# Kernel tuning notes

Hardware: AMD Instinct MI355X
Metric: run time of the kernel (lower is better)

The kernel has to match this reference:

```python
import jax, jax.numpy as jnp
import numpy as np

N = 16384      # total nodes
B = 8          # graphs in batch
NPG = N // B   # nodes per graph
E = 262144     # edges
IN, HID, OUT = 128, 256, 128
ICP_ITERS = 10


def setup_inputs():
    key = jax.random.key(0)
    ks = jax.random.split(key, 12)
    x = jax.random.normal(ks[0], (N, IN), jnp.float32)
    # random edges kept within each graph (offsets per graph)
    src = jax.random.randint(ks[1], (E,), 0, NPG, dtype=jnp.int32)
    dst = jax.random.randint(ks[2], (E,), 0, NPG, dtype=jnp.int32)
    goff = (jnp.arange(E, dtype=jnp.int32) % B) * NPG
    edge_index = jnp.stack([src + goff, dst + goff], 0)
    pos = jax.random.normal(ks[3], (N, 3), jnp.float32)
    batch = jnp.repeat(jnp.arange(B, dtype=jnp.int32), NPG)
    def lin(k, fi, fo):
        return jax.random.normal(k, (fi, fo), jnp.float32) * (fi ** -0.5)
    return dict(
        x=x, edge_index=edge_index, pos=pos, batch=batch,
        W1=lin(ks[4], IN, HID),  b1=jnp.zeros((HID,), jnp.float32),
        W2=lin(ks[5], HID, HID), b2=jnp.zeros((HID,), jnp.float32),
        W3=lin(ks[6], HID, OUT), b3=jnp.zeros((OUT,), jnp.float32),
        Wt=lin(ks[7], OUT, 3),   bt=jnp.zeros((3,), jnp.float32),
    )


def gcn_conv(x, W, b, row, col, n):
    # GCNConv: symmetric norm with self loops; messages flow row->col
    xw = x @ W
    loop = jnp.arange(n, dtype=row.dtype)
    r = jnp.concatenate([row, loop])
    c = jnp.concatenate([col, loop])
    deg = jax.ops.segment_sum(jnp.ones_like(c, dtype=xw.dtype), c, num_segments=n)
    dinv = jnp.where(deg > 0, jax.lax.rsqrt(jnp.maximum(deg, 1e-12)), 0.0)
    norm = dinv[r] * dinv[c]
    out = jax.ops.segment_sum(xw[r] * norm[:, None], c, num_segments=n)
    return out + b


def pdist2(a, b):
    # squared pairwise distances [n,m]
    return (jnp.sum(a * a, -1)[:, None] + jnp.sum(b * b, -1)[None, :]
            - 2.0 * (a @ b.T))


def icp_align(src, tgt):
    # fixed-iteration batched ICP (Kabsch/SVD per iteration)
    for _ in range(ICP_ITERS):
        d = pdist2(jax.lax.stop_gradient(src), jax.lax.stop_gradient(tgt))
        idx = jnp.argmin(d, axis=1)
        corr = tgt[idx]
        cs = jnp.mean(src, 0)
        cc = jnp.mean(corr, 0)
        H = (src - cs).T @ (corr - cc)  # [3,3]
        U, S, Vt = jnp.linalg.svd(H, full_matrices=False)
        sign = jnp.sign(jnp.linalg.det(Vt.T @ U.T))
        D = jnp.stack([jnp.ones_like(sign), jnp.ones_like(sign), sign])
        R = (Vt.T * D[None, :]) @ U.T
        t = cc - R @ cs
        src = src @ R.T + t
    return src


def chamfer(a, b):
    d = pdist2(jax.lax.stop_gradient(a), jax.lax.stop_gradient(b))
    ia = jnp.argmin(d, 1)
    ib = jnp.argmin(d, 0)
    d1 = jnp.mean(jnp.sum((a - b[ia]) ** 2, -1))
    d2 = jnp.mean(jnp.sum((b - a[ib]) ** 2, -1))
    return d1 + d2


def reference(x, edge_index, pos, batch, W1, b1, W2, b2, W3, b3, Wt, bt):
    n = x.shape[0]
    row, col = edge_index[0], edge_index[1]
    h = jax.nn.relu(gcn_conv(x, W1, b1, row, col, n))
    h = jax.nn.relu(gcn_conv(h, W2, b2, row, col, n))
    h = gcn_conv(h, W3, b3, row, col, n)
    pos_offset = h @ Wt + bt
    tpos = pos + pos_offset
    nb = int(batch[-1]) + 1          # sorted, equal-size graphs
    npg = n // nb
    src = tpos.reshape(nb, npg, 3)
    tgt = pos.reshape(nb, npg, 3)
    aligned = jax.vmap(icp_align)(src, tgt)
    loss = jnp.mean(jax.vmap(chamfer)(aligned, tgt))
    return h, aligned.reshape(n, 3), loss
```

## Files before the change

### kernel.cpp

```cpp
#include <hip/hip_runtime.h>
#include <math.h>

#define N_NODES 16384
#define B_GRAPHS 8
#define NPG_     2048
#define E_EDGES  262144
#define F_IN  128
#define F_HID 256
#define F_OUT 128
#define ICP_IT 10
#define NN_BPG 32

typedef __attribute__((ext_vector_type(8))) short bf16x8;
typedef __attribute__((ext_vector_type(4))) float f32x4;

__device__ __forceinline__ float b2f(unsigned short u) {
    union { unsigned int u; float f; } v; v.u = ((unsigned int)u) << 16; return v.f;
}
__device__ __forceinline__ unsigned short f2b(float f) {
    union { float f; unsigned int u; } v; v.f = f;
    unsigned int r = v.u + 0x7FFFu + ((v.u >> 16) & 1u);
    return (unsigned short)(r >> 16);
}
__device__ __forceinline__ int swz32(int i) {
    return (i & ~31) | ((i & 31) ^ ((i >> 5) & 31));
}
__device__ __forceinline__ void st_agent(float* p, float v) {
    __hip_atomic_store(p, v, __ATOMIC_RELAXED, __HIP_MEMORY_SCOPE_AGENT);
}
__device__ __forceinline__ float ld_agent(const float* p) {
    return __hip_atomic_load(p, __ATOMIC_RELAXED, __HIP_MEMORY_SCOPE_AGENT);
}
__device__ __forceinline__ void st_agent_i(int* p, int v) {
    __hip_atomic_store(p, v, __ATOMIC_RELAXED, __HIP_MEMORY_SCOPE_AGENT);
}
__device__ __forceinline__ int ld_agent_i(const int* p) {
    return __hip_atomic_load(p, __ATOMIC_RELAXED, __HIP_MEMORY_SCOPE_AGENT);
}

__global__ __launch_bounds__(256) void k_prep(
    const float* __restrict__ x, unsigned short* __restrict__ xb,
    const float* __restrict__ W1, const float* __restrict__ W2, const float* __restrict__ W3,
    unsigned short* __restrict__ W1b, unsigned short* __restrict__ W2b, unsigned short* __restrict__ W3b,
    const int* __restrict__ col, int* __restrict__ counts)
// ... 44 lines not shown
    __syncthreads();
    if (t < 16) {
        int v = wtot[t];
        for (int o = 1; o < 16; o <<= 1) {
            int u = __shfl_up(v, o);
            if (t >= o) v += u;
        }
        wtot[t] = v;
    }
    __syncthreads();
    int run = (w > 0 ? wtot[w - 1] : 0) + (inc - s);
#pragma unroll
    for (int i = 0; i < 16; i++) {
        offs[base + i]   = run;
        cursor[base + i] = run;
        dinv[base + i]   = rsqrtf((float)(local[i] + 1));
        run += local[i];
    }
    if (t == 1023) offs[N_NODES] = run;
}

__global__ void k_scatter(const int* __restrict__ row, const int* __restrict__ col,
        int* __restrict__ cursor, const float* __restrict__ dinv,
        int* __restrict__ srcid, float* __restrict__ normv)
{
    int e = blockIdx.x * 256 + threadIdx.x;
    if (e >= E_EDGES) return;
    int r = row[e], c = col[e];
    int p = atomicAdd(&cursor[c], 1);
    srcid[p] = r;
    normv[p] = dinv[r] * dinv[c];
}

template<int W, int OUTF, int FUSET>
__global__ __launch_bounds__(128) void k_agg(const unsigned short* __restrict__ X,
        void* __restrict__ Y,
        const int* __restrict__ offs, const int* __restrict__ srcid,
        const float* __restrict__ normv, const float* __restrict__ dinv,
        const float* __restrict__ bias, int relu,
        const float* __restrict__ Wt, const float* __restrict__ bt,
        const float* __restrict__ pos, float* __restrict__ tposO)
{
    constexpr int NPB = (W == 128) ? 2 : 1;
    constexpr int W2 = W / 2;
    const int local = (NPB == 2) ? (threadIdx.x >> 6) : 0;
    const int n = blockIdx.x * NPB + local;
    const int j = (NPB == 2) ? (threadIdx.x & 63) : threadIdx.x;
    const unsigned int* Xu = (const unsigned int*)X;
    float di = dinv[n];
    float w0 = di * di;
    unsigned int v = Xu[(size_t)n * W2 + j];
    float a0 = b2f((unsigned short)v) * w0;
    float a1 = b2f((unsigned short)(v >> 16)) * w0;
    int p = offs[n];
    const int p1 = offs[n + 1];
    for (; p + 3 < p1; p += 4) {
        int s0i = srcid[p], s1i = srcid[p + 1], s2i = srcid[p + 2], s3i = srcid[p + 3];
        float n0 = normv[p], n1 = normv[p + 1], n2 = normv[p + 2], n3 = normv[p + 3];
        unsigned int v0 = Xu[(size_t)s0i * W2 + j];
        unsigned int v1 = Xu[(size_t)s1i * W2 + j];
        unsigned int v2 = Xu[(size_t)s2i * W2 + j];
        unsigned int v3 = Xu[(size_t)s3i * W2 + j];
        a0 = fmaf(b2f((unsigned short)v0), n0, a0);
        a1 = fmaf(b2f((unsigned short)(v0 >> 16)), n0, a1);
        a0 = fmaf(b2f((unsigned short)v1), n1, a0);
        a1 = fmaf(b2f((unsigned short)(v1 >> 16)), n1, a1);
        a0 = fmaf(b2f((unsigned short)v2), n2, a0);
        a1 = fmaf(b2f((unsigned short)(v2 >> 16)), n2, a1);
        a0 = fmaf(b2f((unsigned short)v3), n3, a0);
        a1 = fmaf(b2f((unsigned short)(v3 >> 16)), n3, a1);
    }
    for (; p < p1; ++p) {
        unsigned int va = Xu[(size_t)srcid[p] * W2 + j]; float na = normv[p];
        a0 = fmaf(b2f((unsigned short)va), na, a0);
        a1 = fmaf(b2f((unsigned short)(va >> 16)), na, a1);
    }
    if (bias) { a0 += bias[2 * j]; a1 += bias[2 * j + 1]; }
    if (relu) { a0 = fmaxf(a0, 0.f); a1 = fmaxf(a1, 0.f); }
    if (OUTF) {
        float* Yf = (float*)Y;
        Yf[(size_t)n * W + 2 * j]     = a0;
        Yf[(size_t)n * W + 2 * j + 1] = a1;
    } else {
        ((unsigned int*)Y)[(size_t)n * W2 + j] =
            (unsigned int)f2b(a0) | ((unsigned int)f2b(a1) << 16);
    }
    if (FUSET) {
        float wt0 = Wt[6 * j + 0], wt1 = Wt[6 * j + 1], wt2 = Wt[6 * j + 2];
        float wt3 = Wt[6 * j + 3], wt4 = Wt[6 * j + 4], wt5 = Wt[6 * j + 5];
        float s0 = a0 * wt0 + a1 * wt3;
        float s1 = a0 * wt1 + a1 * wt4;
        float s2 = a0 * wt2 + a1 * wt5;
        for (int o = 32; o > 0; o >>= 1) {
            s0 += __shfl_down(s0, o);
            s1 += __shfl_down(s1, o);
            s2 += __shfl_down(s2, o);
        }
        if (j == 0) {
            tposO[n * 3 + 0] = pos[n * 3 + 0] + s0 + bt[0];
            tposO[n * 3 + 1] = pos[n * 3 + 1] + s1 + bt[1];
            tposO[n * 3 + 2] = pos[n * 3 + 2] + s2 + bt[2];
        }
    }
}

__global__ __launch_bounds__(256) void k_gemm_bf16(
    const unsigned short* __restrict__ A,
    const unsigned short* __restrict__ Bt,
    const float* __restrict__ bias, unsigned short* __restrict__ C,
    int M, int N, int K, int relu)
{
    __shared__ __align__(16) unsigned short As[128 * 64];
    __shared__ __align__(16) unsigned short Bs[64 * 64];
    const int tid  = threadIdx.x;
    const int lane = tid & 63;
    const int wave = tid >> 6;
    const int bm = blockIdx.y * 128, bn = blockIdx.x * 64;
    const int wm = (wave >> 1) * 64, wn = (wave & 1) * 32;
    f32x4 acc[4][2];
#pragma unroll
    for (int mf = 0; mf < 4; mf++)
#pragma unroll
        for (int nf = 0; nf < 2; nf++) acc[mf][nf] = (f32x4){0.f, 0.f, 0.f, 0.f};

    for (int k0 = 0; k0 < K; k0 += 64) {
#pragma unroll
        for (int i = 0; i < 4; i++) {
            int idx = i * 256 + tid;
            int m = idx >> 3, slot = idx & 7;
            const unsigned short* src = A + (size_t)(bm + m) * K + k0 + ((slot ^ (m & 7)) << 3);
            __builtin_amdgcn_global_load_lds(
                (const __attribute__((address_space(1))) unsigned int*)src,
                (__attribute__((address_space(3))) unsigned int*)(As + (size_t)i * 2048 + wave * 512),
                16, 0, 0);
        }
#pragma unroll
// ... 28 lines not shown
        for (int s = 0; s < 2; s++)
#pragma unroll
            for (int mf = 0; mf < 4; mf++)
#pragma unroll
                for (int nf = 0; nf < 2; nf++)
                    acc[mf][nf] = __builtin_amdgcn_mfma_f32_16x16x32_bf16(
                        af[mf][s], bfr[nf][s], acc[mf][nf], 0, 0, 0);
        __syncthreads();
    }
#pragma unroll
    for (int nf = 0; nf < 2; nf++) {
        int col = bn + wn + nf * 16 + (lane & 15);
        float bv = bias ? bias[col] : 0.f;
#pragma unroll
        for (int mf = 0; mf < 4; mf++) {
#pragma unroll
            for (int r = 0; r < 4; r++) {
                int row = bm + wm + mf * 16 + (lane >> 4) * 4 + r;
                float v = acc[mf][nf][r] + bv;
                if (relu) v = fmaxf(v, 0.f);
                C[(size_t)row * N + col] = f2b(v);
            }
        }
    }
}

__global__ __launch_bounds__(512) void k_icp_all(
    const float* __restrict__ tpos, const float* __restrict__ pos,
    float* __restrict__ partials,
    float* __restrict__ chpart,
    int* __restrict__ ctrs,
    float* __restrict__ out_aligned, float* __restrict__ out_loss)
{
    const int g = blockIdx.x >> 5, blk = blockIdx.x & 31;
    const int tid = threadIdx.x;
    const int wave = tid >> 6, lane = tid & 63;
    __shared__ float4 tq[NPG_];
    __shared__ __align__(16) unsigned char scratch[NPG_ * 16];
    float* sm_d = (float*)scratch;
    unsigned short* sm_i = (unsigned short*)(scratch + 64 * 65 * 4);
    float4* al = (float4*)scratch;
    __shared__ float mom[15][33];
    __shared__ float ssx[64], ssy[64], ssz[64];
    __shared__ float wred[8][2];
    __shared__ float Tsh[12];
    __shared__ double sdl[15];
    __shared__ int lastFlag;

    for (int i = tid; i < NPG_; i += 512) {
        const float* p = &pos[(size_t)(g * NPG_ + i) * 3];
        float qx = p[0], qy = p[1], qz = p[2];
        tq[swz32(i)] = make_float4(qx, qy, qz, fmaf(qx, qx, fmaf(qy, qy, qz * qz)));
    }
    if (tid < 12) Tsh[tid] = (tid == 0 || tid == 4 || tid == 8) ? 1.f : 0.f;
    float Px[8], Py[8], Pz[8];
#pragma unroll
    for (int u = 0; u < 8; u++) {
        int n = g * NPG_ + blk * 64 + wave * 8 + u;
        Px[u] = tpos[n * 3 + 0]; Py[u] = tpos[n * 3 + 1]; Pz[u] = tpos[n * 3 + 2];
    }
    double Td[12];
    if (tid == 0) {
#pragma unroll
        for (int k = 0; k < 12; k++) Td[k] = (k == 0 || k == 4 || k == 8) ? 1.0 : 0.0;
    }
    __syncthreads();

    for (int iter = 0; iter < ICP_IT; ++iter) {
        const int bufbase = (iter & 1) * 256;
        float Tf[12];
#pragma unroll
        for (int k = 0; k < 12; k++) Tf[k] = Tsh[k];
        float Sx[8], Sy[8], Sz[8], Tx[8], Ty[8], Tz[8], bd[8];
        int bi[8];
#pragma unroll
        for (int u = 0; u < 8; u++) {
            float X = Tf[0] * Px[u] + Tf[1] * Py[u] + Tf[2] * Pz[u] + Tf[9];
            float Y = Tf[3] * Px[u] + Tf[4] * Py[u] + Tf[5] * Pz[u] + Tf[10];
            float Z = Tf[6] * Px[u] + Tf[7] * Py[u] + Tf[8] * Pz[u] + Tf[11];
            Sx[u] = X; Sy[u] = Y; Sz[u] = Z;
            Tx[u] = -2.f * X; Ty[u] = -2.f * Y; Tz[u] = -2.f * Z;
            bd[u] = 1e30f; bi[u] = lane * 32;
        }
        const int qbase = lane * 32;
        for (int j = 0; j < 32; j++) {
            float4 t4 = tq[qbase + (j ^ (lane & 31))];
            int idx = qbase + j;
#pragma unroll
            for (int u = 0; u < 8; u++) {
                float d = fmaf(Tx[u], t4.x, fmaf(Ty[u], t4.y, fmaf(Tz[u], t4.z, t4.w)));
                if (d < bd[u]) { bd[u] = d; bi[u] = idx; }
            }
        }
#pragma unroll
        for (int u = 0; u < 8; u++) {
            int row = wave * 8 + u;
            sm_d[row * 65 + lane] = bd[u];
            sm_i[row * 65 + lane] = (unsigned short)bi[u];
            if (lane == u) { ssx[row] = Sx[u]; ssy[row] = Sy[u]; ssz[row] = Sz[u]; }
        }
        __syncthreads();
        if (tid < 64) {
            const int s = tid;
            float best = sm_d[s * 65];
            int ib = sm_i[s * 65];
            for (int r = 1; r < 64; r++) {
                float dd = sm_d[s * 65 + r];
                int ii = sm_i[s * 65 + r];
                if (dd < best) { best = dd; ib = ii; }
            }
            float4 c = tq[swz32(ib)];
            float X = ssx[s], Y = ssy[s], Z = ssz[s];
            float vals[15] = { X, Y, Z, c.x, c.y, c.z,
                               X * c.x, X * c.y, X * c.z,
                               Y * c.x, Y * c.y, Y * c.z,
                               Z * c.x, Z * c.y, Z * c.z };
#pragma unroll
            for (int k = 0; k < 15; k++) {
                float v = vals[k];
                for (int o = 32; o > 0; o >>= 1) v += __shfl_down(v, o);
                if (tid == 0) st_agent(&partials[((size_t)bufbase + blockIdx.x) * 16 + k], v);
            }
        }
        __syncthreads();
        if (tid == 0)
            st_agent_i((int*)partials + ((size_t)bufbase + blockIdx.x) * 16 + 15, iter + 1);
        if (tid < 32) {
            const int* tp = (const int*)partials + ((size_t)bufbase + g * 32 + tid) * 16 + 15;
            while (ld_agent_i(tp) < iter + 1) __builtin_amdgcn_s_sleep(1);
        }
        __syncthreads();
        if (tid < 480) {
            int kk = tid >> 5, bb = tid & 31;
            mom[kk][bb] = ld_agent(&partials[((size_t)bufbase + g * 32 + bb) * 16 + kk]);
        }
        __syncthreads();
        if (tid < 15) {
            double acc = 0;
            for (int b = 0; b < NN_BPG; b++) acc += (double)mom[tid][b];
            sdl[tid] = acc;
        }
        __syncthreads();
        if (tid == 0) {
            double sd[15];
#pragma unroll
            for (int k = 0; k < 15; k++) sd[k] = sdl[k];
            const double n = (double)NPG_;
            const double rin = 1.0 / (double)NPG_;
            double cs0 = sd[0] * rin, cs1 = sd[1] * rin, cs2 = sd[2] * rin;
            double cc0 = sd[3] * rin, cc1 = sd[4] * rin, cc2 = sd[5] * rin;
            float H[3][3];
            H[0][0] = (float)(sd[6]  - n * cs0 * cc0); H[0][1] = (float)(sd[7]  - n * cs0 * cc1); H[0][2] = (float)(sd[8]  - n * cs0 * cc2);
            H[1][0] = (float)(sd[9]  - n * cs1 * cc0); H[1][1] = (float)(sd[10] - n * cs1 * cc1); H[1][2] = (float)(sd[11] - n * cs1 * cc2);
            H[2][0] = (float)(sd[12] - n * cs2 * cc0); H[2][1] = (float)(sd[13] - n * cs2 * cc1); H[2][2] = (float)(sd[14] - n * cs2 * cc2);
            double R[3][3];
            float fn = 1e-30f;
            for (int i = 0; i < 3; i++) for (int j2 = 0; j2 < 3; j2++) fn += H[i][j2] * H[i][j2];
            float sc = rsqrtf(fn);
            float Xm[3][3];
            for (int i = 0; i < 3; i++) for (int j2 = 0; j2 < 3; j2++) Xm[i][j2] = H[i][j2] * sc;
            float dX = Xm[0][0] * (Xm[1][1]*Xm[2][2] - Xm[1][2]*Xm[2][1])
                     - Xm[0][1] * (Xm[1][0]*Xm[2][2] - Xm[1][2]*Xm[2][0])
                     + Xm[0][2] * (Xm[1][0]*Xm[2][1] - Xm[1][1]*Xm[2][0]);
            if (dX > 1e-4f) {
                for (int itn = 0; itn < 16; ++itn) {
                    float C00 = Xm[1][1]*Xm[2][2] - Xm[1][2]*Xm[2][1];
                    float C01 = Xm[1][2]*Xm[2][0] - Xm[1][0]*Xm[2][2];
                    float C02 = Xm[1][0]*Xm[2][1] - Xm[1][1]*Xm[2][0];
                    float C10 = Xm[2][1]*Xm[0][2] - Xm[2][2]*Xm[0][1];
                    float C11 = Xm[2][2]*Xm[0][0] - Xm[2][0]*Xm[0][2];
                    float C12 = Xm[2][0]*Xm[0][1] - Xm[2][1]*Xm[0][0];
                    float C20 = Xm[0][1]*Xm[1][2] - Xm[0][2]*Xm[1][1];
                    float C21 = Xm[0][2]*Xm[1][0] - Xm[0][0]*Xm[1][2];
                    float C22 = Xm[0][0]*Xm[1][1] - Xm[0][1]*Xm[1][0];
                    float det = Xm[0][0]*C00 + Xm[0][1]*C01 + Xm[0][2]*C02;
                    if (fabsf(det) < 1e-30f) break;
                    float rd = 0.5f / det;
                    Xm[0][0] = 0.5f*Xm[0][0] + C00*rd; Xm[0][1] = 0.5f*Xm[0][1] + C01*rd; Xm[0][2] = 0.5f*Xm[0][2] + C02*rd;
                    Xm[1][0] = 0.5f*Xm[1][0] + C10*rd; Xm[1][1] = 0.5f*Xm[1][1] + C11*rd; Xm[1][2] = 0.5f*Xm[1][2] + C12*rd;
                    Xm[2][0] = 0.5f*Xm[2][0] + C20*rd; Xm[2][1] = 0.5f*Xm[2][1] + C21*rd; Xm[2][2] = 0.5f*Xm[2][2] + C22*rd;
                }
                for (int i = 0; i < 3; i++) for (int j2 = 0; j2 < 3; j2++) R[i][j2] = (double)Xm[j2][i];
            } else {
                float A[3][3], V[3][3] = {{1,0,0},{0,1,0},{0,0,1}};
                for (int i = 0; i < 3; i++)
                    for (int j2 = 0; j2 < 3; j2++)
                        A[i][j2] = H[0][i] * H[0][j2] + H[1][i] * H[1][j2] + H[2][i] * H[2][j2];
                for (int sweep = 0; sweep < 8; ++sweep) {
                    for (int p = 0; p < 2; p++) for (int q = p + 1; q < 3; q++) {
                        float apq = A[p][q];
                        if (fabsf(apq) < 1e-30f) continue;
                        float theta = (A[q][q] - A[p][p]) / (2.f * apq);
                        float t = copysignf(1.f, theta) / (fabsf(theta) + sqrtf(theta * theta + 1.f));
                        float c = 1.f / sqrtf(t * t + 1.f);
                        float s = t * c;
                        for (int k = 0; k < 3; k++) { float akp = A[k][p], akq = A[k][q]; A[k][p] = c*akp - s*akq; A[k][q] = s*akp + c*akq; }
                        for (int k = 0; k < 3; k++) { float apk = A[p][k], aqk = A[q][k]; A[p][k] = c*apk - s*aqk; A[q][k] = s*apk + c*aqk; }
                        for (int k = 0; k < 3; k++) { float vkp = V[k][p], vkq = V[k][q]; V[k][p] = c*vkp - s*vkq; V[k][q] = s*vkp + c*vkq; }
                    }
                }
                float lam[3] = { A[0][0], A[1][1], A[2][2] };
                int ord[3] = { 0, 1, 2 };
                if (lam[ord[1]] > lam[ord[0]]) { int t0 = ord[0]; ord[0] = ord[1]; ord[1] = t0; }
                if (lam[ord[2]] > lam[ord[0]]) { int t0 = ord[0]; ord[0] = ord[2]; ord[2] = t0; }
                if (lam[ord[2]] > lam[ord[1]]) { int t0 = ord[1]; ord[1] = ord[2]; ord[2] = t0; }
                float vc[3][3], uc[3][3];
                for (int i = 0; i < 3; i++) { vc[i][0] = V[0][ord[i]]; vc[i][1] = V[1][ord[i]]; vc[i][2] = V[2][ord[i]]; }
                for (int i = 0; i < 3; i++) {
                    float u0 = H[0][0]*vc[i][0] + H[0][1]*vc[i][1] + H[0][2]*vc[i][2];
                    float u1 = H[1][0]*vc[i][0] + H[1][1]*vc[i][1] + H[1][2]*vc[i][2];
                    float u2 = H[2][0]*vc[i][0] + H[2][1]*vc[i][1] + H[2][2]*vc[i][2];
                    for (int j2 = 0; j2 < i; j2++) {
                        float dp = u0*uc[j2][0] + u1*uc[j2][1] + u2*uc[j2][2];
                        u0 -= dp*uc[j2][0]; u1 -= dp*uc[j2][1]; u2 -= dp*uc[j2][2];
                    }
                    float nn2 = sqrtf(u0*u0 + u1*u1 + u2*u2);
                    if (nn2 > 1e-12f) { uc[i][0] = u0/nn2; uc[i][1] = u1/nn2; uc[i][2] = u2/nn2; }
                    else if (i == 2) {
                        uc[2][0] = uc[0][1]*uc[1][2] - uc[0][2]*uc[1][1];
                        uc[2][1] = uc[0][2]*uc[1][0] - uc[0][0]*uc[1][2];
                        uc[2][2] = uc[0][0]*uc[1][1] - uc[0][1]*uc[1][0];
                    } else if (i == 1) {
                        float a0 = (fabsf(uc[0][0]) < 0.9f) ? 1.f : 0.f, a1 = 1.f - a0, a2 = 0.f;
                        float dp = a0*uc[0][0] + a1*uc[0][1] + a2*uc[0][2];
                        a0 -= dp*uc[0][0]; a1 -= dp*uc[0][1]; a2 -= dp*uc[0][2];
                        float nn3 = sqrtf(a0*a0 + a1*a1 + a2*a2);
                        uc[1][0] = a0/nn3; uc[1][1] = a1/nn3; uc[1][2] = a2/nn3;
                    } else { uc[0][0] = 1; uc[0][1] = 0; uc[0][2] = 0; }
                }
                float detU = uc[0][0]*(uc[1][1]*uc[2][2] - uc[1][2]*uc[2][1])
                           - uc[0][1]*(uc[1][0]*uc[2][2] - uc[1][2]*uc[2][0])
                           + uc[0][2]*(uc[1][0]*uc[2][1] - uc[1][1]*uc[2][0]);
                float detV = vc[0][0]*(vc[1][1]*vc[2][2] - vc[1][2]*vc[2][1])
                           - vc[0][1]*(vc[1][0]*vc[2][2] - vc[1][2]*vc[2][0])
                           + vc[0][2]*(vc[1][0]*vc[2][1] - vc[1][1]*vc[2][0]);
                float sgn = (detU * detV < 0.f) ? -1.f : 1.f;
                for (int i = 0; i < 3; i++)
                    for (int j2 = 0; j2 < 3; j2++)
                        R[i][j2] = (double)(vc[0][i]*uc[0][j2] + vc[1][i]*uc[1][j2] + sgn * vc[2][i]*uc[2][j2]);
            }
            double tr0 = cc0 - (R[0][0]*cs0 + R[0][1]*cs1 + R[0][2]*cs2);
            double tr1 = cc1 - (R[1][0]*cs0 + R[1][1]*cs1 + R[1][2]*cs2);
            double tr2 = cc2 - (R[2][0]*cs0 + R[2][1]*cs1 + R[2][2]*cs2);
            double An[12];
            for (int i = 0; i < 3; i++)
                for (int j2 = 0; j2 < 3; j2++)
                    An[i*3+j2] = R[i][0]*Td[0*3+j2] + R[i][1]*Td[1*3+j2] + R[i][2]*Td[2*3+j2];
            An[9]  = R[0][0]*Td[9] + R[0][1]*Td[10] + R[0][2]*Td[11] + tr0;
            An[10] = R[1][0]*Td[9] + R[1][1]*Td[10] + R[1][2]*Td[11] + tr1;
            An[11] = R[2][0]*Td[9] + R[2][1]*Td[10] + R[2][2]*Td[11] + tr2;
#pragma unroll
            for (int k = 0; k < 12; k++) { Td[k] = An[k]; Tsh[k] = (float)An[k]; }
        }
        __syncthreads();
    }

    {
        float Tf[12];
#pragma unroll
        for (int k = 0; k < 12; k++) Tf[k] = Tsh[k];
        __syncthreads();
        for (int i = tid; i < NPG_; i += 512) {
            const float* q = &tpos[(size_t)(g * NPG_ + i) * 3];
            float X = Tf[0] * q[0] + Tf[1] * q[1] + Tf[2] * q[2] + Tf[9];
            float Y = Tf[3] * q[0] + Tf[4] * q[1] + Tf[5] * q[2] + Tf[10];
            float Z = Tf[6] * q[0] + Tf[7] * q[1] + Tf[8] * q[2] + Tf[11];
            al[swz32(i)] = make_float4(X, Y, Z, fmaf(X, X, fmaf(Y, Y, Z * Z)));
            if (blk == 0) {
                out_aligned[(size_t)(g * NPG_ + i) * 3 + 0] = X;
                out_aligned[(size_t)(g * NPG_ + i) * 3 + 1] = Y;
                out_aligned[(size_t)(g * NPG_ + i) * 3 + 2] = Z;
            }
        }
        __syncthreads();
        float Ax[8], Ay[8], Az[8], Aw[8], Qx[8], Qy[8], Qz[8], Qw[8], d1[8], d2[8];
#pragma unroll
        for (int u = 0; u < 8; u++) {
            int s = swz32(blk * 64 + wave * 8 + u);
            float4 a4 = al[s]; float4 p4 = tq[s];
            Ax[u] = -2.f * a4.x; Ay[u] = -2.f * a4.y; Az[u] = -2.f * a4.z; Aw[u] = a4.w;
            Qx[u] = -2.f * p4.x; Qy[u] = -2.f * p4.y; Qz[u] = -2.f * p4.z; Qw[u] = p4.w;
            d1[u] = 1e30f; d2[u] = 1e30f;
        }
        const int qbase = lane * 32;
        for (int j = 0; j < 32; j++) {
// ... 76 lines not shown
    size_t off_b = 0;
    auto alloc = [&](size_t bytes) -> void* {
        void* p = wsb + off_b;
        off_b = (off_b + bytes + 255) & ~(size_t)255;
        return p;
    };
    int*    counts   = (int*)alloc((size_t)N_NODES * 4);
    float*  partials = (float*)alloc((size_t)2 * 256 * 16 * 4);
    int*    ctrs     = (int*)alloc((size_t)256 * 4);
    int*    offs     = (int*)alloc((size_t)(N_NODES + 1) * 4);
    int*    cursor   = (int*)alloc((size_t)N_NODES * 4);
    int*    srcid    = (int*)alloc((size_t)E_EDGES * 4);
    float*  normv    = (float*)alloc((size_t)E_EDGES * 4);
    float*  dinv     = (float*)alloc((size_t)N_NODES * 4);
    unsigned short* xb  = (unsigned short*)alloc((size_t)N_NODES * F_IN * 2);
    unsigned short* W1b = (unsigned short*)alloc((size_t)F_IN * F_HID * 2);
    unsigned short* W2b = (unsigned short*)alloc((size_t)F_HID * F_HID * 2);
    unsigned short* W3b = (unsigned short*)alloc((size_t)F_HID * F_OUT * 2);
    unsigned short* bufA = (unsigned short*)alloc((size_t)N_NODES * F_HID * 2);
    unsigned short* bufB = (unsigned short*)alloc((size_t)N_NODES * F_HID * 2);
    unsigned short* bufC = (unsigned short*)alloc((size_t)N_NODES * F_HID * 2);
    float*  tpos     = (float*)alloc((size_t)N_NODES * 3 * 4);
    float*  chpart   = (float*)alloc((size_t)256 * 2 * 4);

    float* out_h       = (float*)d_out;
    float* out_aligned = out_h + (size_t)N_NODES * F_OUT;
    float* out_loss    = out_aligned + (size_t)N_NODES * 3;

    hipMemsetAsync(counts, 0, (size_t)N_NODES * 4 + 2 * 256 * 16 * 4 + 256 * 4, stream);
    k_prep<<<3584, 256, 0, stream>>>(x, xb, W1, W2, W3, W1b, W2b, W3b, col, counts);
    k_scan<<<1, 1024, 0, stream>>>(counts, offs, cursor, dinv);
    k_scatter<<<E_EDGES / 256, 256, 0, stream>>>(row, col, cursor, dinv, srcid, normv);

    k_agg<F_IN, 0, 0><<<N_NODES / 2, 128, 0, stream>>>(xb, bufA, offs, srcid, normv, dinv,
            nullptr, 0, nullptr, nullptr, nullptr, nullptr);
    {
        dim3 grid(F_HID / 64, N_NODES / 128);
        k_gemm_bf16<<<grid, 256, 0, stream>>>(bufA, W1b, b1, bufB, N_NODES, F_HID, F_IN, 1);
    }
    {
        dim3 grid(F_HID / 64, N_NODES / 128);
        k_gemm_bf16<<<grid, 256, 0, stream>>>(bufB, W2b, nullptr, bufC, N_NODES, F_HID, F_HID, 0);
    }
    k_agg<F_HID, 0, 0><<<N_NODES, 128, 0, stream>>>(bufC, bufA, offs, srcid, normv, dinv,
            b2, 1, nullptr, nullptr, nullptr, nullptr);
    {
        dim3 grid(F_OUT / 64, N_NODES / 128);
        k_gemm_bf16<<<grid, 256, 0, stream>>>(bufA, W3b, nullptr, bufB, N_NODES, F_OUT, F_HID, 0);
    }
    k_agg<F_OUT, 1, 1><<<N_NODES / 2, 128, 0, stream>>>(bufB, out_h, offs, srcid, normv, dinv,
            b3, 0, Wt, bt, pos, tpos);

    k_icp_all<<<B_GRAPHS * NN_BPG, 512, 0, stream>>>(tpos, pos, partials, chpart, ctrs,
            out_aligned, out_loss);
}
```

Baseline: 308.8 us.

## Vectorize 256-wide aggregation and streamline ICP cross-block moment reduction

Adds a dedicated 256-feature aggregation kernel in which each wave handles one node with 8-byte loads (4 bf16 per lane), two nodes per block. The 256-wide layer previously used one node per 128-thread block with 4-byte loads. In the ICP kernel, wave 0 alone now publishes its partial moments, spins on the per-block flags, reduces the 32 partials with wave shuffles in double, and solves the rotation. This replaces several block-wide barriers and the shared-memory moment tables. Block-to-graph mapping is interleaved so the blocks of one graph spread across the device, at the cost of relying on co-residency for the spin-wait.

```diff
diff --git a/kernel.cpp b/kernel.cpp
--- a/kernel.cpp
+++ b/kernel.cpp
@@ -9,7 +9,6 @@
 #define F_HID 256
 #define F_OUT 128
 #define ICP_IT 10
-#define NN_BPG 32
 
 typedef __attribute__((ext_vector_type(8))) short bf16x8;
 typedef __attribute__((ext_vector_type(4))) float f32x4;
@@ -120,8 +119,8 @@
     normv[p] = dinv[r] * dinv[c];
 }
 
-template<int W, int OUTF, int FUSET>
-__global__ __launch_bounds__(128) void k_agg(const unsigned short* __restrict__ X,
+template<int OUTF, int FUSET>
+__global__ __launch_bounds__(128) void k_agg128(const unsigned short* __restrict__ X,
         void* __restrict__ Y,
         const int* __restrict__ offs, const int* __restrict__ srcid,
         const float* __restrict__ normv, const float* __restrict__ dinv,
@@ -129,15 +128,13 @@
         const float* __restrict__ Wt, const float* __restrict__ bt,
         const float* __restrict__ pos, float* __restrict__ tposO)
 {
-    constexpr int NPB = (W == 128) ? 2 : 1;
-    constexpr int W2 = W / 2;
-    const int local = (NPB == 2) ? (threadIdx.x >> 6) : 0;
-    const int n = blockIdx.x * NPB + local;
-    const int j = (NPB == 2) ? (threadIdx.x & 63) : threadIdx.x;
+    const int local = threadIdx.x >> 6;
+    const int n = blockIdx.x * 2 + local;
+    const int j = threadIdx.x & 63;
     const unsigned int* Xu = (const unsigned int*)X;
     float di = dinv[n];
     float w0 = di * di;
-    unsigned int v = Xu[(size_t)n * W2 + j];
+    unsigned int v = Xu[(size_t)n * 64 + j];
     float a0 = b2f((unsigned short)v) * w0;
     float a1 = b2f((unsigned short)(v >> 16)) * w0;
     int p = offs[n];
@@ -145,10 +142,10 @@
     for (; p + 3 < p1; p += 4) {
         int s0i = srcid[p], s1i = srcid[p + 1], s2i = srcid[p + 2], s3i = srcid[p + 3];
         float n0 = normv[p], n1 = normv[p + 1], n2 = normv[p + 2], n3 = normv[p + 3];
-        unsigned int v0 = Xu[(size_t)s0i * W2 + j];
-        unsigned int v1 = Xu[(size_t)s1i * W2 + j];
-        unsigned int v2 = Xu[(size_t)s2i * W2 + j];
-        unsigned int v3 = Xu[(size_t)s3i * W2 + j];
+        unsigned int v0 = Xu[(size_t)s0i * 64 + j];
+        unsigned int v1 = Xu[(size_t)s1i * 64 + j];
+        unsigned int v2 = Xu[(size_t)s2i * 64 + j];
+        unsigned int v3 = Xu[(size_t)s3i * 64 + j];
         a0 = fmaf(b2f((unsigned short)v0), n0, a0);
         a1 = fmaf(b2f((unsigned short)(v0 >> 16)), n0, a1);
         a0 = fmaf(b2f((unsigned short)v1), n1, a0);
@@ -159,7 +156,7 @@
         a1 = fmaf(b2f((unsigned short)(v3 >> 16)), n3, a1);
     }
     for (; p < p1; ++p) {
-        unsigned int va = Xu[(size_t)srcid[p] * W2 + j]; float na = normv[p];
+        unsigned int va = Xu[(size_t)srcid[p] * 64 + j]; float na = normv[p];
         a0 = fmaf(b2f((unsigned short)va), na, a0);
         a1 = fmaf(b2f((unsigned short)(va >> 16)), na, a1);
     }
@@ -167,10 +164,10 @@
     if (relu) { a0 = fmaxf(a0, 0.f); a1 = fmaxf(a1, 0.f); }
     if (OUTF) {
         float* Yf = (float*)Y;
-        Yf[(size_t)n * W + 2 * j]     = a0;
-        Yf[(size_t)n * W + 2 * j + 1] = a1;
+        Yf[(size_t)n * 128 + 2 * j]     = a0;
+        Yf[(size_t)n * 128 + 2 * j + 1] = a1;
     } else {
-        ((unsigned int*)Y)[(size_t)n * W2 + j] =
+        ((unsigned int*)Y)[(size_t)n * 64 + j] =
             (unsigned int)f2b(a0) | ((unsigned int)f2b(a1) << 16);
     }
     if (FUSET) {
@@ -190,6 +187,70 @@
             tposO[n * 3 + 2] = pos[n * 3 + 2] + s2 + bt[2];
         }
     }
+}
+
+__global__ __launch_bounds__(128) void k_agg256(const unsigned short* __restrict__ X,
+        unsigned short* __restrict__ Y,
+        const int* __restrict__ offs, const int* __restrict__ srcid,
+        const float* __restrict__ normv, const float* __restrict__ dinv,
+        const float* __restrict__ bias, int relu)
+{
+    const int local = threadIdx.x >> 6;
+    const int n = blockIdx.x * 2 + local;
+    const int lane = threadIdx.x & 63;
+    const uint2* Xu = (const uint2*)X;
+    float di = dinv[n];
+    float w0 = di * di;
+    uint2 v = Xu[(size_t)n * 64 + lane];
+    float a0 = b2f((unsigned short)v.x) * w0;
+    float a1 = b2f((unsigned short)(v.x >> 16)) * w0;
+    float a2 = b2f((unsigned short)v.y) * w0;
+    float a3 = b2f((unsigned short)(v.y >> 16)) * w0;
+    int p = offs[n];
+    const int p1 = offs[n + 1];
+    for (; p + 3 < p1; p += 4) {
+        int s0i = srcid[p], s1i = srcid[p + 1], s2i = srcid[p + 2], s3i = srcid[p + 3];
+        float n0 = normv[p], n1 = normv[p + 1], n2 = normv[p + 2], n3 = normv[p + 3];
+        uint2 v0 = Xu[(size_t)s0i * 64 + lane];
+        uint2 v1 = Xu[(size_t)s1i * 64 + lane];
+        uint2 v2 = Xu[(size_t)s2i * 64 + lane];
+        uint2 v3 = Xu[(size_t)s3i * 64 + lane];
+        a0 = fmaf(b2f((unsigned short)v0.x), n0, a0);
+        a1 = fmaf(b2f((unsigned short)(v0.x >> 16)), n0, a1);
+        a2 = fmaf(b2f((unsigned short)v0.y), n0, a2);
+        a3 = fmaf(b2f((unsigned short)(v0.y >> 16)), n0, a3);
+        a0 = fmaf(b2f((unsigned short)v1.x), n1, a0);
+        a1 = fmaf(b2f((unsigned short)(v1.x >> 16)), n1, a1);
+        a2 = fmaf(b2f((unsigned short)v1.y), n1, a2);
+        a3 = fmaf(b2f((unsigned short)(v1.y >> 16)), n1, a3);
+        a0 = fmaf(b2f((unsigned short)v2.x), n2, a0);
+        a1 = fmaf(b2f((unsigned short)(v2.x >> 16)), n2, a1);
+        a2 = fmaf(b2f((unsigned short)v2.y), n2, a2);
+        a3 = fmaf(b2f((unsigned short)(v2.y >> 16)), n2, a3);
+        a0 = fmaf(b2f((unsigned short)v3.x), n3, a0);
+        a1 = fmaf(b2f((unsigned short)(v3.x >> 16)), n3, a1);
+        a2 = fmaf(b2f((unsigned short)v3.y), n3, a2);
+        a3 = fmaf(b2f((unsigned short)(v3.y >> 16)), n3, a3);
+    }
+    for (; p < p1; ++p) {
+        uint2 va = Xu[(size_t)srcid[p] * 64 + lane]; float na = normv[p];
+        a0 = fmaf(b2f((unsigned short)va.x), na, a0);
+        a1 = fmaf(b2f((unsigned short)(va.x >> 16)), na, a1);
+        a2 = fmaf(b2f((unsigned short)va.y), na, a2);
+        a3 = fmaf(b2f((unsigned short)(va.y >> 16)), na, a3);
+    }
+    if (bias) {
+        float4 bv = ((const float4*)bias)[lane];
+        a0 += bv.x; a1 += bv.y; a2 += bv.z; a3 += bv.w;
+    }
+    if (relu) {
+        a0 = fmaxf(a0, 0.f); a1 = fmaxf(a1, 0.f);
+        a2 = fmaxf(a2, 0.f); a3 = fmaxf(a3, 0.f);
+    }
+    uint2 o;
+    o.x = (unsigned int)f2b(a0) | ((unsigned int)f2b(a1) << 16);
+    o.y = (unsigned int)f2b(a2) | ((unsigned int)f2b(a3) << 16);
+    ((uint2*)Y)[(size_t)n * 64 + lane] = o;
 }
 
 __global__ __launch_bounds__(256) void k_gemm_bf16(
@@ -284,7 +345,8 @@
     int* __restrict__ ctrs,
     float* __restrict__ out_aligned, float* __restrict__ out_loss)
 {
-    const int g = blockIdx.x >> 5, blk = blockIdx.x & 31;
+    const int g = blockIdx.x & 7, blk = blockIdx.x >> 3;
+    const int myline = g * 32 + blk;
     const int tid = threadIdx.x;
     const int wave = tid >> 6, lane = tid & 63;
     __shared__ float4 tq[NPG_];
@@ -292,11 +354,9 @@
     float* sm_d = (float*)scratch;
     unsigned short* sm_i = (unsigned short*)(scratch + 64 * 65 * 4);
     float4* al = (float4*)scratch;
-    __shared__ float mom[15][33];
     __shared__ float ssx[64], ssy[64], ssz[64];
     __shared__ float wred[8][2];
     __shared__ float Tsh[12];
-    __shared__ double sdl[15];
     __shared__ int lastFlag;
 
     for (int i = tid; i < NPG_; i += 512) {
@@ -352,7 +412,7 @@
             if (lane == u) { ssx[row] = Sx[u]; ssy[row] = Sy[u]; ssz[row] = Sz[u]; }
         }
         __syncthreads();
-        if (tid < 64) {
+        if (wave == 0) {
             const int s = tid;
             float best = sm_d[s * 65];
             int ib = sm_i[s * 65];
@@ -371,138 +431,134 @@
             for (int k = 0; k < 15; k++) {
                 float v = vals[k];
                 for (int o = 32; o > 0; o >>= 1) v += __shfl_down(v, o);
-                if (tid == 0) st_agent(&partials[((size_t)bufbase + blockIdx.x) * 16 + k], v);
-            }
-        }
-        __syncthreads();
-        if (tid == 0)
-            st_agent_i((int*)partials + ((size_t)bufbase + blockIdx.x) * 16 + 15, iter + 1);
-        if (tid < 32) {
-            const int* tp = (const int*)partials + ((size_t)bufbase + g * 32 + tid) * 16 + 15;
-            while (ld_agent_i(tp) < iter + 1) __builtin_amdgcn_s_sleep(1);
-        }
-        __syncthreads();
-        if (tid < 480) {
-            int kk = tid >> 5, bb = tid & 31;
-            mom[kk][bb] = ld_agent(&partials[((size_t)bufbase + g * 32 + bb) * 16 + kk]);
-        }
-        __syncthreads();
-        if (tid < 15) {
-            double acc = 0;
-            for (int b = 0; b < NN_BPG; b++) acc += (double)mom[tid][b];
-            sdl[tid] = acc;
-        }
-        __syncthreads();
-        if (tid == 0) {
+                if (lane == 0) st_agent(&partials[((size_t)bufbase + myline) * 16 + k], v);
+            }
+            if (lane == 0) {
+                asm volatile("s_waitcnt vmcnt(0)" ::: "memory");
+                st_agent_i((int*)partials + ((size_t)bufbase + myline) * 16 + 15, iter + 1);
+            }
             double sd[15];
 #pragma unroll
-            for (int k = 0; k < 15; k++) sd[k] = sdl[k];
-            const double n = (double)NPG_;
-            const double rin = 1.0 / (double)NPG_;
-            double cs0 = sd[0] * rin, cs1 = sd[1] * rin, cs2 = sd[2] * rin;
-            double cc0 = sd[3] * rin, cc1 = sd[4] * rin, cc2 = sd[5] * rin;
-            float H[3][3];
-            H[0][0] = (float)(sd[6]  - n * cs0 * cc0); H[0][1] = (float)(sd[7]  - n * cs0 * cc1); H[0][2] = (float)(sd[8]  - n * cs0 * cc2);
-            H[1][0] = (float)(sd[9]  - n * cs1 * cc0); H[1][1] = (float)(sd[10] - n * cs1 * cc1); H[1][2] = (float)(sd[11] - n * cs1 * cc2);
-            H[2][0] = (float)(sd[12] - n * cs2 * cc0); H[2][1] = (float)(sd[13] - n * cs2 * cc1); H[2][2] = (float)(sd[14] - n * cs2 * cc2);
-            double R[3][3];
-            float fn = 1e-30f;
-            for (int i = 0; i < 3; i++) for (int j2 = 0; j2 < 3; j2++) fn += H[i][j2] * H[i][j2];
-            float sc = rsqrtf(fn);
-            float Xm[3][3];
-            for (int i = 0; i < 3; i++) for (int j2 = 0; j2 < 3; j2++) Xm[i][j2] = H[i][j2] * sc;
-            float dX = Xm[0][0] * (Xm[1][1]*Xm[2][2] - Xm[1][2]*Xm[2][1])
-                     - Xm[0][1] * (Xm[1][0]*Xm[2][2] - Xm[1][2]*Xm[2][0])
-                     + Xm[0][2] * (Xm[1][0]*Xm[2][1] - Xm[1][1]*Xm[2][0]);
-            if (dX > 1e-4f) {
-                for (int itn = 0; itn < 16; ++itn) {
-                    float C00 = Xm[1][1]*Xm[2][2] - Xm[1][2]*Xm[2][1];
-                    float C01 = Xm[1][2]*Xm[2][0] - Xm[1][0]*Xm[2][2];
-                    float C02 = Xm[1][0]*Xm[2][1] - Xm[1][1]*Xm[2][0];
-                    float C10 = Xm[2][1]*Xm[0][2] - Xm[2][2]*Xm[0][1];
-                    float C11 = Xm[2][2]*Xm[0][0] - Xm[2][0]*Xm[0][2];
-                    float C12 = Xm[2][0]*Xm[0][1] - Xm[2][1]*Xm[0][0];
-                    float C20 = Xm[0][1]*Xm[1][2] - Xm[0][2]*Xm[1][1];
-                    float C21 = Xm[0][2]*Xm[1][0] - Xm[0][0]*Xm[1][2];
-                    float C22 = Xm[0][0]*Xm[1][1] - Xm[0][1]*Xm[1][0];
-                    float det = Xm[0][0]*C00 + Xm[0][1]*C01 + Xm[0][2]*C02;
-                    if (fabsf(det) < 1e-30f) break;
-                    float rd = 0.5f / det;
-                    Xm[0][0] = 0.5f*Xm[0][0] + C00*rd; Xm[0][1] = 0.5f*Xm[0][1] + C01*rd; Xm[0][2] = 0.5f*Xm[0][2] + C02*rd;
-                    Xm[1][0] = 0.5f*Xm[1][0] + C10*rd; Xm[1][1] = 0.5f*Xm[1][1] + C11*rd; Xm[1][2] = 0.5f*Xm[1][2] + C12*rd;
-                    Xm[2][0] = 0.5f*Xm[2][0] + C20*rd; Xm[2][1] = 0.5f*Xm[2][1] + C21*rd; Xm[2][2] = 0.5f*Xm[2][2] + C22*rd;
+            for (int k = 0; k < 15; k++) sd[k] = 0.0;
+            if (lane < 32) {
+                const float* lp = partials + ((size_t)bufbase + g * 32 + lane) * 16;
+                while (ld_agent_i((const int*)lp + 15) < iter + 1) __builtin_amdgcn_s_sleep(1);
+                asm volatile("" ::: "memory");
+#pragma unroll
+                for (int k = 0; k < 15; k++) sd[k] = (double)ld_agent(lp + k);
+            }
+#pragma unroll
+            for (int k = 0; k < 15; k++) {
+                for (int o = 16; o > 0; o >>= 1) sd[k] += __shfl_down(sd[k], o);
+            }
+            if (lane == 0) {
+                const double n = (double)NPG_;
+                const double rin = 1.0 / (double)NPG_;
+                double cs0 = sd[0] * rin, cs1 = sd[1] * rin, cs2 = sd[2] * rin;
+                double cc0 = sd[3] * rin, cc1 = sd[4] * rin, cc2 = sd[5] * rin;
+                float H[3][3];
+                H[0][0] = (float)(sd[6]  - n * cs0 * cc0); H[0][1] = (float)(sd[7]  - n * cs0 * cc1); H[0][2] = (float)(sd[8]  - n * cs0 * cc2);
+                H[1][0] = (float)(sd[9]  - n * cs1 * cc0); H[1][1] = (float)(sd[10] - n * cs1 * cc1); H[1][2] = (float)(sd[11] - n * cs1 * cc2);
+                H[2][0] = (float)(sd[12] - n * cs2 * cc0); H[2][1] = (float)(sd[13] - n * cs2 * cc1); H[2][2] = (float)(sd[14] - n * cs2 * cc2);
+                double R[3][3];
+                float fn = 1e-30f;
+                for (int i = 0; i < 3; i++) for (int j2 = 0; j2 < 3; j2++) fn += H[i][j2] * H[i][j2];
+                float sc = rsqrtf(fn);
+                float Xm[3][3];
+                for (int i = 0; i < 3; i++) for (int j2 = 0; j2 < 3; j2++) Xm[i][j2] = H[i][j2] * sc;
+                float dX = Xm[0][0] * (Xm[1][1]*Xm[2][2] - Xm[1][2]*Xm[2][1])
+                         - Xm[0][1] * (Xm[1][0]*Xm[2][2] - Xm[1][2]*Xm[2][0])
+                         + Xm[0][2] * (Xm[1][0]*Xm[2][1] - Xm[1][1]*Xm[2][0]);
+                if (dX > 1e-4f) {
+                    for (int itn = 0; itn < 16; ++itn) {
+                        float C00 = Xm[1][1]*Xm[2][2] - Xm[1][2]*Xm[2][1];
+                        float C01 = Xm[1][2]*Xm[2][0] - Xm[1][0]*Xm[2][2];
+                        float C02 = Xm[1][0]*Xm[2][1] - Xm[1][1]*Xm[2][0];
+                        float C10 = Xm[2][1]*Xm[0][2] - Xm[2][2]*Xm[0][1];
+                        float C11 = Xm[2][2]*Xm[0][0] - Xm[2][0]*Xm[0][2];
+                        float C12 = Xm[2][0]*Xm[0][1] - Xm[2][1]*Xm[0][0];
+                        float C20 = Xm[0][1]*Xm[1][2] - Xm[0][2]*Xm[1][1];
+                        float C21 = Xm[0][2]*Xm[1][0] - Xm[0][0]*Xm[1][2];
+                        float C22 = Xm[0][0]*Xm[1][1] - Xm[0][1]*Xm[1][0];
+                        float det = Xm[0][0]*C00 + Xm[0][1]*C01 + Xm[0][2]*C02;
+                        if (fabsf(det) < 1e-30f) break;
+                        float rd = 0.5f / det;
+                        Xm[0][0] = 0.5f*Xm[0][0] + C00*rd; Xm[0][1] = 0.5f*Xm[0][1] + C01*rd; Xm[0][2] = 0.5f*Xm[0][2] + C02*rd;
+                        Xm[1][0] = 0.5f*Xm[1][0] + C10*rd; Xm[1][1] = 0.5f*Xm[1][1] + C11*rd; Xm[1][2] = 0.5f*Xm[1][2] + C12*rd;
+                        Xm[2][0] = 0.5f*Xm[2][0] + C20*rd; Xm[2][1] = 0.5f*Xm[2][1] + C21*rd; Xm[2][2] = 0.5f*Xm[2][2] + C22*rd;
+                    }
+                    for (int i = 0; i < 3; i++) for (int j2 = 0; j2 < 3; j2++) R[i][j2] = (double)Xm[j2][i];
+                } else {
+                    float A[3][3], V[3][3] = {{1,0,0},{0,1,0},{0,0,1}};
+                    for (int i = 0; i < 3; i++)
+                        for (int j2 = 0; j2 < 3; j2++)
+                            A[i][j2] = H[0][i] * H[0][j2] + H[1][i] * H[1][j2] + H[2][i] * H[2][j2];
+                    for (int sweep = 0; sweep < 8; ++sweep) {
+                        for (int p = 0; p < 2; p++) for (int q = p + 1; q < 3; q++) {
+                            float apq = A[p][q];
+                            if (fabsf(apq) < 1e-30f) continue;
+                            float theta = (A[q][q] - A[p][p]) / (2.f * apq);
+                            float t = copysignf(1.f, theta) / (fabsf(theta) + sqrtf(theta * theta + 1.f));
+                            float c2 = 1.f / sqrtf(t * t + 1.f);
+                            float s2 = t * c2;
+                            for (int k = 0; k < 3; k++) { float akp = A[k][p], akq = A[k][q]; A[k][p] = c2*akp - s2*akq; A[k][q] = s2*akp + c2*akq; }
+                            for (int k = 0; k < 3; k++) { float apk = A[p][k], aqk = A[q][k]; A[p][k] = c2*apk - s2*aqk; A[q][k] = s2*apk + c2*aqk; }
+                            for (int k = 0; k < 3; k++) { float vkp = V[k][p], vkq = V[k][q]; V[k][p] = c2*vkp - s2*vkq; V[k][q] = s2*vkp + c2*vkq; }
+                        }
+                    }
+                    float lam[3] = { A[0][0], A[1][1], A[2][2] };
+                    int ord[3] = { 0, 1, 2 };
+                    if (lam[ord[1]] > lam[ord[0]]) { int t0 = ord[0]; ord[0] = ord[1]; ord[1] = t0; }
+                    if (lam[ord[2]] > lam[ord[0]]) { int t0 = ord[0]; ord[0] = ord[2]; ord[2] = t0; }
+                    if (lam[ord[2]] > lam[ord[1]]) { int t0 = ord[1]; ord[1] = ord[2]; ord[2] = t0; }
+                    float vc[3][3], uc[3][3];
+                    for (int i = 0; i < 3; i++) { vc[i][0] = V[0][ord[i]]; vc[i][1] = V[1][ord[i]]; vc[i][2] = V[2][ord[i]]; }
+                    for (int i = 0; i < 3; i++) {
+                        float u0 = H[0][0]*vc[i][0] + H[0][1]*vc[i][1] + H[0][2]*vc[i][2];
+                        float u1 = H[1][0]*vc[i][0] + H[1][1]*vc[i][1] + H[1][2]*vc[i][2];
+                        float u2 = H[2][0]*vc[i][0] + H[2][1]*vc[i][1] + H[2][2]*vc[i][2];
+                        for (int j2 = 0; j2 < i; j2++) {
+                            float dp = u0*uc[j2][0] + u1*uc[j2][1] + u2*uc[j2][2];
+                            u0 -= dp*uc[j2][0]; u1 -= dp*uc[j2][1]; u2 -= dp*uc[j2][2];
+                        }
+                        float nn2 = sqrtf(u0*u0 + u1*u1 + u2*u2);
+                        if (nn2 > 1e-12f) { uc[i][0] = u0/nn2; uc[i][1] = u1/nn2; uc[i][2] = u2/nn2; }
+                        else if (i == 2) {
+                            uc[2][0] = uc[0][1]*uc[1][2] - uc[0][2]*uc[1][1];
+                            uc[2][1] = uc[0][2]*uc[1][0] - uc[0][0]*uc[1][2];
+                            uc[2][2] = uc[0][0]*uc[1][1] - uc[0][1]*uc[1][0];
+                        } else if (i == 1) {
+                            float a0 = (fabsf(uc[0][0]) < 0.9f) ? 1.f : 0.f, a1 = 1.f - a0, a2 = 0.f;
+                            float dp = a0*uc[0][0] + a1*uc[0][1] + a2*uc[0][2];
+                            a0 -= dp*uc[0][0]; a1 -= dp*uc[0][1]; a2 -= dp*uc[0][2];
+                            float nn3 = sqrtf(a0*a0 + a1*a1 + a2*a2);
+                            uc[1][0] = a0/nn3; uc[1][1] = a1/nn3; uc[1][2] = a2/nn3;
+                        } else { uc[0][0] = 1; uc[0][1] = 0; uc[0][2] = 0; }
+                    }
+                    float detU = uc[0][0]*(uc[1][1]*uc[2][2] - uc[1][2]*uc[2][1])
+                               - uc[0][1]*(uc[1][0]*uc[2][2] - uc[1][2]*uc[2][0])
+                               + uc[0][2]*(uc[1][0]*uc[2][1] - uc[1][1]*uc[2][0]);
+                    float detV = vc[0][0]*(vc[1][1]*vc[2][2] - vc[1][2]*vc[2][1])
+                               - vc[0][1]*(vc[1][0]*vc[2][2] - vc[1][2]*vc[2][0])
+                               + vc[0][2]*(vc[1][0]*vc[2][1] - vc[1][1]*vc[2][0]);
+                    float sgn = (detU * detV < 0.f) ? -1.f : 1.f;
+                    for (int i = 0; i < 3; i++)
+                        for (int j2 = 0; j2 < 3; j2++)
+                            R[i][j2] = (double)(vc[0][i]*uc[0][j2] + vc[1][i]*uc[1][j2] + sgn * vc[2][i]*uc[2][j2]);
                 }
-                for (int i = 0; i < 3; i++) for (int j2 = 0; j2 < 3; j2++) R[i][j2] = (double)Xm[j2][i];
-            } else {
-                float A[3][3], V[3][3] = {{1,0,0},{0,1,0},{0,0,1}};
+                double tr0 = cc0 - (R[0][0]*cs0 + R[0][1]*cs1 + R[0][2]*cs2);
+                double tr1 = cc1 - (R[1][0]*cs0 + R[1][1]*cs1 + R[1][2]*cs2);
+                double tr2 = cc2 - (R[2][0]*cs0 + R[2][1]*cs1 + R[2][2]*cs2);
+                double An[12];
                 for (int i = 0; i < 3; i++)
                     for (int j2 = 0; j2 < 3; j2++)
-                        A[i][j2] = H[0][i] * H[0][j2] + H[1][i] * H[1][j2] + H[2][i] * H[2][j2];
-                for (int sweep = 0; sweep < 8; ++sweep) {
-                    for (int p = 0; p < 2; p++) for (int q = p + 1; q < 3; q++) {
-                        float apq = A[p][q];
-                        if (fabsf(apq) < 1e-30f) continue;
-                        float theta = (A[q][q] - A[p][p]) / (2.f * apq);
-                        float t = copysignf(1.f, theta) / (fabsf(theta) + sqrtf(theta * theta + 1.f));
-                        float c = 1.f / sqrtf(t * t + 1.f);
-                        float s = t * c;
-                        for (int k = 0; k < 3; k++) { float akp = A[k][p], akq = A[k][q]; A[k][p] = c*akp - s*akq; A[k][q] = s*akp + c*akq; }
-                        for (int k = 0; k < 3; k++) { float apk = A[p][k], aqk = A[q][k]; A[p][k] = c*apk - s*aqk; A[q][k] = s*apk + c*aqk; }
-                        for (int k = 0; k < 3; k++) { float vkp = V[k][p], vkq = V[k][q]; V[k][p] = c*vkp - s*vkq; V[k][q] = s*vkp + c*vkq; }
-                    }
-                }
-                float lam[3] = { A[0][0], A[1][1], A[2][2] };
-                int ord[3] = { 0, 1, 2 };
-                if (lam[ord[1]] > lam[ord[0]]) { int t0 = ord[0]; ord[0] = ord[1]; ord[1] = t0; }
-                if (lam[ord[2]] > lam[ord[0]]) { int t0 = ord[0]; ord[0] = ord[2]; ord[2] = t0; }
-                if (lam[ord[2]] > lam[ord[1]]) { int t0 = ord[1]; ord[1] = ord[2]; ord[2] = t0; }
-                float vc[3][3], uc[3][3];
-                for (int i = 0; i < 3; i++) { vc[i][0] = V[0][ord[i]]; vc[i][1] = V[1][ord[i]]; vc[i][2] = V[2][ord[i]]; }
-                for (int i = 0; i < 3; i++) {
-                    float u0 = H[0][0]*vc[i][0] + H[0][1]*vc[i][1] + H[0][2]*vc[i][2];
-                    float u1 = H[1][0]*vc[i][0] + H[1][1]*vc[i][1] + H[1][2]*vc[i][2];
-                    float u2 = H[2][0]*vc[i][0] + H[2][1]*vc[i][1] + H[2][2]*vc[i][2];
-                    for (int j2 = 0; j2 < i; j2++) {
-                        float dp = u0*uc[j2][0] + u1*uc[j2][1] + u2*uc[j2][2];
-                        u0 -= dp*uc[j2][0]; u1 -= dp*uc[j2][1]; u2 -= dp*uc[j2][2];
-                    }
-                    float nn2 = sqrtf(u0*u0 + u1*u1 + u2*u2);
-                    if (nn2 > 1e-12f) { uc[i][0] = u0/nn2; uc[i][1] = u1/nn2; uc[i][2] = u2/nn2; }
-                    else if (i == 2) {
-                        uc[2][0] = uc[0][1]*uc[1][2] - uc[0][2]*uc[1][1];
-                        uc[2][1] = uc[0][2]*uc[1][0] - uc[0][0]*uc[1][2];
-                        uc[2][2] = uc[0][0]*uc[1][1] - uc[0][1]*uc[1][0];
-                    } else if (i == 1) {
-                        float a0 = (fabsf(uc[0][0]) < 0.9f) ? 1.f : 0.f, a1 = 1.f - a0, a2 = 0.f;
-                        float dp = a0*uc[0][0] + a1*uc[0][1] + a2*uc[0][2];
-                        a0 -= dp*uc[0][0]; a1 -= dp*uc[0][1]; a2 -= dp*uc[0][2];
-                        float nn3 = sqrtf(a0*a0 + a1*a1 + a2*a2);
-                        uc[1][0] = a0/nn3; uc[1][1] = a1/nn3; uc[1][2] = a2/nn3;
-                    } else { uc[0][0] = 1; uc[0][1] = 0; uc[0][2] = 0; }
-                }
-                float detU = uc[0][0]*(uc[1][1]*uc[2][2] - uc[1][2]*uc[2][1])
-                           - uc[0][1]*(uc[1][0]*uc[2][2] - uc[1][2]*uc[2][0])
-                           + uc[0][2]*(uc[1][0]*uc[2][1] - uc[1][1]*uc[2][0]);
-                float detV = vc[0][0]*(vc[1][1]*vc[2][2] - vc[1][2]*vc[2][1])
-                           - vc[0][1]*(vc[1][0]*vc[2][2] - vc[1][2]*vc[2][0])
-                           + vc[0][2]*(vc[1][0]*vc[2][1] - vc[1][1]*vc[2][0]);
-                float sgn = (detU * detV < 0.f) ? -1.f : 1.f;
-                for (int i = 0; i < 3; i++)
-                    for (int j2 = 0; j2 < 3; j2++)
-                        R[i][j2] = (double)(vc[0][i]*uc[0][j2] + vc[1][i]*uc[1][j2] + sgn * vc[2][i]*uc[2][j2]);
-            }
-            double tr0 = cc0 - (R[0][0]*cs0 + R[0][1]*cs1 + R[0][2]*cs2);
-            double tr1 = cc1 - (R[1][0]*cs0 + R[1][1]*cs1 + R[1][2]*cs2);
-            double tr2 = cc2 - (R[2][0]*cs0 + R[2][1]*cs1 + R[2][2]*cs2);
-            double An[12];
-            for (int i = 0; i < 3; i++)
-                for (int j2 = 0; j2 < 3; j2++)
-                    An[i*3+j2] = R[i][0]*Td[0*3+j2] + R[i][1]*Td[1*3+j2] + R[i][2]*Td[2*3+j2];
-            An[9]  = R[0][0]*Td[9] + R[0][1]*Td[10] + R[0][2]*Td[11] + tr0;
-            An[10] = R[1][0]*Td[9] + R[1][1]*Td[10] + R[1][2]*Td[11] + tr1;
-            An[11] = R[2][0]*Td[9] + R[2][1]*Td[10] + R[2][2]*Td[11] + tr2;
-#pragma unroll
-            for (int k = 0; k < 12; k++) { Td[k] = An[k]; Tsh[k] = (float)An[k]; }
+                        An[i*3+j2] = R[i][0]*Td[0*3+j2] + R[i][1]*Td[1*3+j2] + R[i][2]*Td[2*3+j2];
+                An[9]  = R[0][0]*Td[9] + R[0][1]*Td[10] + R[0][2]*Td[11] + tr0;
+                An[10] = R[1][0]*Td[9] + R[1][1]*Td[10] + R[1][2]*Td[11] + tr1;
+                An[11] = R[2][0]*Td[9] + R[2][1]*Td[10] + R[2][2]*Td[11] + tr2;
+#pragma unroll
+                for (int k = 0; k < 12; k++) { Td[k] = An[k]; Tsh[k] = (float)An[k]; }
+            }
         }
         __syncthreads();
     }
@@ -645,7 +701,7 @@
     k_scan<<<1, 1024, 0, stream>>>(counts, offs, cursor, dinv);
     k_scatter<<<E_EDGES / 256, 256, 0, stream>>>(row, col, cursor, dinv, srcid, normv);
 
-    k_agg<F_IN, 0, 0><<<N_NODES / 2, 128, 0, stream>>>(xb, bufA, offs, srcid, normv, dinv,
+    k_agg128<0, 0><<<N_NODES / 2, 128, 0, stream>>>(xb, bufA, offs, srcid, normv, dinv,
             nullptr, 0, nullptr, nullptr, nullptr, nullptr);
     {
         dim3 grid(F_HID / 64, N_NODES / 128);
@@ -655,15 +711,14 @@
         dim3 grid(F_HID / 64, N_NODES / 128);
         k_gemm_bf16<<<grid, 256, 0, stream>>>(bufB, W2b, nullptr, bufC, N_NODES, F_HID, F_HID, 0);
     }
-    k_agg<F_HID, 0, 0><<<N_NODES, 128, 0, stream>>>(bufC, bufA, offs, srcid, normv, dinv,
-            b2, 1, nullptr, nullptr, nullptr, nullptr);
+    k_agg256<<<N_NODES / 2, 128, 0, stream>>>(bufC, bufA, offs, srcid, normv, dinv, b2, 1);
     {
         dim3 grid(F_OUT / 64, N_NODES / 128);
         k_gemm_bf16<<<grid, 256, 0, stream>>>(bufA, W3b, nullptr, bufB, N_NODES, F_OUT, F_HID, 0);
     }
-    k_agg<F_OUT, 1, 1><<<N_NODES / 2, 128, 0, stream>>>(bufB, out_h, offs, srcid, normv, dinv,
+    k_agg128<1, 1><<<N_NODES / 2, 128, 0, stream>>>(bufB, out_h, offs, srcid, normv, dinv,
             b3, 0, Wt, bt, pos, tpos);
 
-    k_icp_all<<<B_GRAPHS * NN_BPG, 512, 0, stream>>>(tpos, pos, partials, chpart, ctrs,
+    k_icp_all<<<256, 512, 0, stream>>>(tpos, pos, partials, chpart, ctrs,
             out_aligned, out_loss);
 }
```

Measured after the change: 322.4 us. 1.04x slower.
